# Kernel tuning notes

Hardware: AMD Instinct MI355X
Metric: run time of the kernel (lower is better)

The kernel has to match this reference:

```python
import jax, jax.numpy as jnp
import numpy as np

B, D, H, FPL, L, LOG2_T = 65536, 768, 512, 4, 16, 19
T = 2 ** LOG2_T
BASE_RES, FINEST_RES = 16, 512
PRIMES = jnp.array([1, 2654435761, 805459861], dtype=jnp.uint32)


def setup_inputs() -> dict:
    key = jax.random.key(0)
    ks = jax.random.split(key, 8)
    t = jax.random.uniform(ks[0], (B,), dtype=jnp.float32)
    x = jax.random.normal(ks[1], (B, D), dtype=jnp.float32)
    cond = jax.random.uniform(ks[2], (B, 2), dtype=jnp.float32)
    # one embedding table per level, Instant-NGP init U(-1e-4, 1e-4)
    tables = jax.random.uniform(ks[3], (L, T, FPL), dtype=jnp.float32,
                                minval=-1e-4, maxval=1e-4)
    in_dim = D + L * FPL  # 832

    def lin(k, fan_in, fan_out):
        return jax.random.normal(k, (fan_in, fan_out), dtype=jnp.float32) / np.sqrt(fan_in).astype(np.float32)

    W0, b0 = lin(ks[4], in_dim, H), jnp.zeros((H,), jnp.float32)
    W1, b1 = lin(ks[5], H, H), jnp.zeros((H,), jnp.float32)
    W2, b2 = lin(ks[6], H, H), jnp.zeros((H,), jnp.float32)
    W3, b3 = lin(ks[7], H, D), jnp.zeros((D,), jnp.float32)
    return dict(t=t, x=x, cond=cond, tables=tables,
                W0=W0, b0=b0, W1=W1, b1=b1, W2=W2, b2=b2, W3=W3, b3=b3)


def hash_encode(coords, tables):
    """coords: [B,3] in [0,1]; tables: [L,T,F] -> [B, L*F]."""
    Ln, Tn, Fn = tables.shape
    growth = np.exp((np.log(FINEST_RES) - np.log(BASE_RES)) / (Ln - 1))
    scales = jnp.asarray(np.floor(BASE_RES * growth ** np.arange(Ln)),
                         dtype=coords.dtype)                      # [L]
    xf = coords[:, None, :] * scales[None, :, None]               # [B,L,3]
    xl = jnp.floor(xf)
    w = xf - xl                                                   # [B,L,3] trilinear frac
    xi = xl.astype(jnp.uint32)
    # 8 cube-corner offsets
    offs = jnp.asarray(np.stack(np.meshgrid([0, 1], [0, 1], [0, 1],
                                            indexing='ij'), -1).reshape(8, 3),
                       dtype=jnp.uint32)                          # [8,3]
    corners = xi[:, :, None, :] + offs[None, None]                # [B,L,8,3]
    h = corners * PRIMES                                          # uint32 wraparound hash
    idx = (h[..., 0] ^ h[..., 1] ^ h[..., 2]) & jnp.uint32(Tn - 1)  # [B,L,8]
    feats = tables[jnp.arange(Ln)[None, :, None], idx]            # [B,L,8,F] gather
    offs_f = offs.astype(coords.dtype)
    wc = jnp.prod(jnp.where(offs_f[None, None] == 1,
                            w[:, :, None, :], 1 - w[:, :, None, :]), axis=-1)  # [B,L,8]
    out = jnp.einsum('blc,blcf->blf', wc, feats)                  # [B,L,F]
    return out.reshape(out.shape[0], Ln * Fn)


def reference(t, x, cond, tables, W0, b0, W1, b1, W2, b2, W3, b3):
    tcol = t[:, None] if t.ndim == 1 else t
    params3 = jnp.concatenate([cond, tcol], axis=-1)   # [B,3]
    enc = hash_encode(params3, tables)                  # [B,64]
    h = jnp.concatenate([x, enc], axis=-1)              # [B,832]
    h = jax.nn.silu(h @ W0 + b0)
    h = jax.nn.silu(h @ W1 + b1)
    h = jax.nn.silu(h @ W2 + b2)
    return h @ W3 + b3                                  # [B,768]
```

## Files before the change

kernel.cpp:

```cpp
#include <hip/hip_runtime.h>
#include <hip/hip_bf16.h>
#include <math.h>


#define T_SIZE 524288
#define T_MASK (T_SIZE - 1)

typedef _Float16 f16;
typedef _Float16 f16x8 __attribute__((ext_vector_type(8)));
typedef _Float16 f16x4 __attribute__((ext_vector_type(4)));
typedef float f32x4 __attribute__((ext_vector_type(4)));

struct Scales { float s[16]; };

__global__ void wfrag(const float* __restrict__ W, f16* __restrict__ Wf, int K, int N) {
  int tid = blockIdx.x * 256 + threadIdx.x;
  int lane = tid & 63, frag = tid >> 6;
  int KS = K >> 5;
  int nblk = frag / KS, ks = frag - nblk * KS;
  if (nblk * 16 >= N) return;
  int n = nblk * 16 + (lane & 15);
  int kb = ks * 32 + (lane >> 4) * 8;
  f16x8 v;
#pragma unroll
  for (int j = 0; j < 8; ++j) v[j] = (f16)W[(size_t)(kb + j) * N + n];
  *(f16x8*)(Wf + (size_t)frag * 512 + lane * 8) = v;
}

__device__ __forceinline__ float silu_f(float v) {
  return v * __builtin_amdgcn_rcpf(1.f + __expf(-v));
}

__global__ __launch_bounds__(512, 2) void fused_mlp(
    const float* __restrict__ x, const float* __restrict__ t,
    const float* __restrict__ cond, const float* __restrict__ tables,
    const f16* __restrict__ Wf0, const f16* __restrict__ Wf1,
    const f16* __restrict__ Wf2, const f16* __restrict__ Wf3,
    const float* __restrict__ b0, const float* __restrict__ b1,
    const float* __restrict__ b2, const float* __restrict__ b3,
    float* __restrict__ out, Scales scl) {
  __shared__ f16 act[128 * 512];
  __shared__ f16 stg[2 * 128 * 32];

  const int tid = threadIdx.x;
  const int wave = tid >> 6, lane = tid & 63;
  const int l16 = lane & 15, lhi = lane >> 4;
  const int rowBase = blockIdx.x * 128;
  const int sr = tid >> 2, sc = tid & 3;
  const int woff = sr * 32 + 8 * (sc ^ ((sr >> 1) & 3));

  f16x8 er24, er25;
  {
    int row = rowBase + sr;
    float c0 = cond[2 * row], c1 = cond[2 * row + 1], c2 = t[row];
#pragma unroll
    for (int h = 0; h < 2; ++h) {
      f16x8 er;
#pragma unroll
      for (int d = 0; d < 2; ++d) {
        int l = h * 8 + sc * 2 + d;
        float s = scl.s[l];
        float xf0 = c0 * s, xf1 = c1 * s, xf2 = c2 * s;
        float xl0 = floorf(xf0), xl1 = floorf(xf1), xl2 = floorf(xf2);
        float w0 = xf0 - xl0, w1 = xf1 - xl1, w2 = xf2 - xl2;
        unsigned xi0 = (unsigned)xl0, xi1 = (unsigned)xl1, xi2 = (unsigned)xl2;
        const float4* tl = (const float4*)tables + (size_t)l * T_SIZE;
        float a0 = 0.f, a1 = 0.f, a2 = 0.f, a3 = 0.f;
#pragma unroll
        for (int c = 0; c < 8; ++c) {
          unsigned ax = (c >> 2) & 1u, ay = (c >> 1) & 1u, az = c & 1u;
          unsigned hh = (xi0 + ax) ^ ((xi1 + ay) * 2654435761u) ^ ((xi2 + az) * 805459861u);
          float4 f = tl[hh & T_MASK];
          float wcw = (ax ? w0 : 1.f - w0) * (ay ? w1 : 1.f - w1) * (az ? w2 : 1.f - w2);
          a0 += wcw * f.x; a1 += wcw * f.y; a2 += wcw * f.z; a3 += wcw * f.w;
        }
        er[d * 4 + 0] = (f16)a0; er[d * 4 + 1] = (f16)a1;
        er[d * 4 + 2] = (f16)a2; er[d * 4 + 3] = (f16)a3;
      }
      if (h == 0) er24 = er; else er25 = er;
    }
  }

  f32x4 acc[8][4];
  f16x8 bfA[4], bfB[4], af[8];

#pragma unroll
  for (int mi = 0; mi < 8; ++mi)
#pragma unroll
    for (int ni = 0; ni < 4; ++ni) acc[mi][ni] = (f32x4){0.f, 0.f, 0.f, 0.f};

  {
    const float* xp = x + (size_t)(rowBase + sr) * 768 + sc * 8;
    float4 a = *(const float4*)xp, b = *(const float4*)(xp + 4);
    f16x8 v = { (f16)a.x, (f16)a.y, (f16)a.z, (f16)a.w,
                (f16)b.x, (f16)b.y, (f16)b.z, (f16)b.w };
    *(f16x8*)(stg + woff) = v;
  }
#pragma unroll
  for (int ni = 0; ni < 4; ++ni)
    bfA[ni] = *(const f16x8*)(Wf0 + ((size_t)(wave * 4 + ni) * 26) * 512 + lane * 8);
  __syncthreads();

#pragma unroll 1
  for (int ks = 0; ks < 26; ++ks) {
    const int nxt = ks + 1;
    f16x8 nv;
    if (nxt < 24) {
      const float* xp = x + (size_t)(rowBase + sr) * 768 + nxt * 32 + sc * 8;
      float4 a = *(const float4*)xp, b = *(const float4*)(xp + 4);
      nv = (f16x8){ (f16)a.x, (f16)a.y, (f16)a.z, (f16)a.w,
                    (f16)b.x, (f16)b.y, (f16)b.z, (f16)b.w };
    } else {
      nv = (nxt == 24) ? er24 : er25;
    }
    if (nxt < 26) {
#pragma unroll
      for (int ni = 0; ni < 4; ++ni)
        bfB[ni] = *(const f16x8*)(Wf0 + ((size_t)(wave * 4 + ni) * 26 + nxt) * 512 + lane * 8);
    }
    const int rb = (ks & 1) * 4096;
#pragma unroll
    for (int mi = 0; mi < 8; ++mi) {
      int r = mi * 16 + l16;
      af[mi] = *(const f16x8*)(stg + rb + r * 32 + 8 * (lhi ^ ((r >> 1) & 3)));
    }
    __builtin_amdgcn_s_setprio(1);
#pragma unroll
    for (int mi = 0; mi < 8; ++mi)
#pragma unroll
      for (int ni = 0; ni < 4; ++ni)
        acc[mi][ni] = __builtin_amdgcn_mfma_f32_16x16x32_f16(bfA[ni], af[mi], acc[mi][ni], 0, 0, 0);
    __builtin_amdgcn_s_setprio(0);
    if (nxt < 26) {
      *(f16x8*)(stg + (nxt & 1) * 4096 + woff) = nv;
#pragma unroll
      for (int ni = 0; ni < 4; ++ni) bfA[ni] = bfB[ni];
    }
    __syncthreads();
  }

  auto epi_act = [&](const float* __restrict__ bias) {
    __syncthreads();
#pragma unroll
    for (int mi = 0; mi < 8; ++mi) {
      const int row = mi * 16 + l16;
#pragma unroll
      for (int ni = 0; ni < 4; ++ni) {
        const int col = wave * 64 + ni * 16 + lhi * 4;
        float4 bv = *(const float4*)(bias + col);
        f16x4 o;
        o[0] = (f16)silu_f(acc[mi][ni][0] + bv.x);
        o[1] = (f16)silu_f(acc[mi][ni][1] + bv.y);
        o[2] = (f16)silu_f(acc[mi][ni][2] + bv.z);
        o[3] = (f16)silu_f(acc[mi][ni][3] + bv.w);
        *(f16x4*)(act + row * 512 + (col ^ ((row & 7) << 3))) = o;
      }
    }
    __syncthreads();
  };
  epi_act(b0);

  auto kloop4 = [&](const f16* __restrict__ Wf) {
#pragma unroll
    for (int mi = 0; mi < 8; ++mi)
#pragma unroll
      for (int ni = 0; ni < 4; ++ni) acc[mi][ni] = (f32x4){0.f, 0.f, 0.f, 0.f};
#pragma unroll
    for (int ni = 0; ni < 4; ++ni)
      bfA[ni] = *(const f16x8*)(Wf + ((size_t)(wave * 4 + ni) * 16) * 512 + lane * 8);
#pragma unroll 1
    for (int ks = 0; ks < 16; ++ks) {
      if (ks < 15) {
#pragma unroll
        for (int ni = 0; ni < 4; ++ni)
          bfB[ni] = *(const f16x8*)(Wf + ((size_t)(wave * 4 + ni) * 16 + ks + 1) * 512 + lane * 8);
      }
#pragma unroll
      for (int mi = 0; mi < 8; ++mi) {
        int r = mi * 16 + l16;
        af[mi] = *(const f16x8*)(act + r * 512 + ((ks * 32 + lhi * 8) ^ ((r & 7) << 3)));
      }
      __builtin_amdgcn_s_setprio(1);
#pragma unroll
      for (int mi = 0; mi < 8; ++mi)
#pragma unroll
        for (int ni = 0; ni < 4; ++ni)
          acc[mi][ni] = __builtin_amdgcn_mfma_f32_16x16x32_f16(bfA[ni], af[mi], acc[mi][ni], 0, 0, 0);
      __builtin_amdgcn_s_setprio(0);
      if (ks < 15) {
#pragma unroll
        for (int ni = 0; ni < 4; ++ni) bfA[ni] = bfB[ni];
      }
    }
  };

  kloop4(Wf1); epi_act(b1);
  kloop4(Wf2); epi_act(b2);

  kloop4(Wf3);
#pragma unroll
  for (int mi = 0; mi < 8; ++mi) {
    const size_t row = (size_t)(rowBase + mi * 16 + l16);
#pragma unroll
    for (int ni = 0; ni < 4; ++ni) {
      const int col = wave * 64 + ni * 16 + lhi * 4;
      float4 bv = *(const float4*)(b3 + col);
      float4 o = { acc[mi][ni][0] + bv.x, acc[mi][ni][1] + bv.y,
                   acc[mi][ni][2] + bv.z, acc[mi][ni][3] + bv.w };
      *(float4*)(out + row * 768 + col) = o;
    }
  }

#pragma unroll
  for (int mi = 0; mi < 8; ++mi)
#pragma unroll
    for (int ni = 0; ni < 2; ++ni) acc[mi][ni] = (f32x4){0.f, 0.f, 0.f, 0.f};
#pragma unroll
  for (int ni = 0; ni < 2; ++ni)
    bfA[ni] = *(const f16x8*)(Wf3 + ((size_t)(32 + wave * 2 + ni) * 16) * 512 + lane * 8);
#pragma unroll 1
  for (int ks = 0; ks < 16; ++ks) {
    if (ks < 15) {
#pragma unroll
      for (int ni = 0; ni < 2; ++ni)
        bfB[ni] = *(const f16x8*)(Wf3 + ((size_t)(32 + wave * 2 + ni) * 16 + ks + 1) * 512 + lane * 8);
    }
#pragma unroll
    for (int mi = 0; mi < 8; ++mi) {
      int r = mi * 16 + l16;
      af[mi] = *(const f16x8*)(act + r * 512 + ((ks * 32 + lhi * 8) ^ ((r & 7) << 3)));
    }
    __builtin_amdgcn_s_setprio(1);
#pragma unroll
    for (int mi = 0; mi < 8; ++mi)
#pragma unroll
      for (int ni = 0; ni < 2; ++ni)
        acc[mi][ni] = __builtin_amdgcn_mfma_f32_16x16x32_f16(bfA[ni], af[mi], acc[mi][ni], 0, 0, 0);
    __builtin_amdgcn_s_setprio(0);
    if (ks < 15) {
#pragma unroll
      for (int ni = 0; ni < 2; ++ni) bfA[ni] = bfB[ni];
    }
  }
#pragma unroll
  for (int mi = 0; mi < 8; ++mi) {
    const size_t row = (size_t)(rowBase + mi * 16 + l16);
#pragma unroll
    for (int ni = 0; ni < 2; ++ni) {
      const int col = 512 + wave * 32 + ni * 16 + lhi * 4;
      float4 bv = *(const float4*)(b3 + col);
      float4 o = { acc[mi][ni][0] + bv.x, acc[mi][ni][1] + bv.y,
                   acc[mi][ni][2] + bv.z, acc[mi][ni][3] + bv.w };
      *(float4*)(out + row * 768 + col) = o;
    }
  }
}

extern "C" void kernel_launch(void* const* d_in, const int* in_sizes, int n_in,
                              void* d_out, int out_size, void* d_ws, size_t ws_size,
                              hipStream_t stream) {
  const float* t    = (const float*)d_in[0];
  const float* x    = (const float*)d_in[1];
  const float* cond = (const float*)d_in[2];
  const float* tab  = (const float*)d_in[3];
  const float* W0   = (const float*)d_in[4];
  const float* b0   = (const float*)d_in[5];
  const float* W1   = (const float*)d_in[6];
  const float* b1   = (const float*)d_in[7];
  const float* W2   = (const float*)d_in[8];
  const float* b2   = (const float*)d_in[9];
  const float* W3   = (const float*)d_in[10];
  const float* b3   = (const float*)d_in[11];
  float* out = (float*)d_out;
  (void)in_sizes; (void)n_in; (void)out_size; (void)ws_size;

  char* ws = (char*)d_ws;
  f16* Wf0 = (f16*)(ws + 0);
  f16* Wf1 = (f16*)(ws + 851968);
  f16* Wf2 = (f16*)(ws + 1376256);
  f16* Wf3 = (f16*)(ws + 1900544);

  wfrag<<<dim3(208), 256, 0, stream>>>(W0, Wf0, 832, 512);
  wfrag<<<dim3(128), 256, 0, stream>>>(W1, Wf1, 512, 512);
  wfrag<<<dim3(128), 256, 0, stream>>>(W2, Wf2, 512, 512);
  wfrag<<<dim3(192), 256, 0, stream>>>(W3, Wf3, 512, 768);

  Scales sc;
  {
    double growth = exp((log(512.0) - log(16.0)) / 15.0);
    for (int l = 0; l < 16; ++l) sc.s[l] = (float)floor(16.0 * pow(growth, (double)l));
  }

  fused_mlp<<<dim3(512), 512, 0, stream>>>(x, t, cond, tab, Wf0, Wf1, Wf2, Wf3,
                                           b0, b1, b2, b3, out, sc);
}
```

Measured before the change: 305.2 us.

## Halve row tile to 64 per block to double grid and occupancy

```diff
diff --git a/kernel.cpp b/kernel.cpp
--- a/kernel.cpp
+++ b/kernel.cpp
@@ -31,7 +31,7 @@
   return v * __builtin_amdgcn_rcpf(1.f + __expf(-v));
 }
 
-__global__ __launch_bounds__(512, 2) void fused_mlp(
+__global__ __launch_bounds__(512, 4) void fused_mlp(
     const float* __restrict__ x, const float* __restrict__ t,
     const float* __restrict__ cond, const float* __restrict__ tables,
     const f16* __restrict__ Wf0, const f16* __restrict__ Wf1,
@@ -39,62 +39,54 @@
     const float* __restrict__ b0, const float* __restrict__ b1,
     const float* __restrict__ b2, const float* __restrict__ b3,
     float* __restrict__ out, Scales scl) {
-  __shared__ f16 act[128 * 512];
-  __shared__ f16 stg[2 * 128 * 32];
+  __shared__ f16 act[64 * 512];
+  __shared__ f16 stg[2 * 64 * 40];
 
   const int tid = threadIdx.x;
   const int wave = tid >> 6, lane = tid & 63;
   const int l16 = lane & 15, lhi = lane >> 4;
-  const int rowBase = blockIdx.x * 128;
-  const int sr = tid >> 2, sc = tid & 3;
-  const int woff = sr * 32 + 8 * (sc ^ ((sr >> 1) & 3));
-
-  f16x8 er24, er25;
+  const int rowBase = blockIdx.x * 64;
+  const int sr = tid >> 3, sc = tid & 7;
+
+  f16x4 er_a, er_b;
   {
     int row = rowBase + sr;
     float c0 = cond[2 * row], c1 = cond[2 * row + 1], c2 = t[row];
 #pragma unroll
     for (int h = 0; h < 2; ++h) {
-      f16x8 er;
-#pragma unroll
-      for (int d = 0; d < 2; ++d) {
-        int l = h * 8 + sc * 2 + d;
-        float s = scl.s[l];
-        float xf0 = c0 * s, xf1 = c1 * s, xf2 = c2 * s;
-        float xl0 = floorf(xf0), xl1 = floorf(xf1), xl2 = floorf(xf2);
-        float w0 = xf0 - xl0, w1 = xf1 - xl1, w2 = xf2 - xl2;
-        unsigned xi0 = (unsigned)xl0, xi1 = (unsigned)xl1, xi2 = (unsigned)xl2;
-        const float4* tl = (const float4*)tables + (size_t)l * T_SIZE;
-        float a0 = 0.f, a1 = 0.f, a2 = 0.f, a3 = 0.f;
-#pragma unroll
-        for (int c = 0; c < 8; ++c) {
-          unsigned ax = (c >> 2) & 1u, ay = (c >> 1) & 1u, az = c & 1u;
-          unsigned hh = (xi0 + ax) ^ ((xi1 + ay) * 2654435761u) ^ ((xi2 + az) * 805459861u);
-          float4 f = tl[hh & T_MASK];
-          float wcw = (ax ? w0 : 1.f - w0) * (ay ? w1 : 1.f - w1) * (az ? w2 : 1.f - w2);
-          a0 += wcw * f.x; a1 += wcw * f.y; a2 += wcw * f.z; a3 += wcw * f.w;
-        }
-        er[d * 4 + 0] = (f16)a0; er[d * 4 + 1] = (f16)a1;
-        er[d * 4 + 2] = (f16)a2; er[d * 4 + 3] = (f16)a3;
-      }
-      if (h == 0) er24 = er; else er25 = er;
-    }
-  }
-
-  f32x4 acc[8][4];
-  f16x8 bfA[4], bfB[4], af[8];
-
-#pragma unroll
-  for (int mi = 0; mi < 8; ++mi)
+      int l = sc + h * 8;
+      float s = scl.s[l];
+      float xf0 = c0 * s, xf1 = c1 * s, xf2 = c2 * s;
+      float xl0 = floorf(xf0), xl1 = floorf(xf1), xl2 = floorf(xf2);
+      float w0 = xf0 - xl0, w1 = xf1 - xl1, w2 = xf2 - xl2;
+      unsigned xi0 = (unsigned)xl0, xi1 = (unsigned)xl1, xi2 = (unsigned)xl2;
+      const float4* tl = (const float4*)tables + (size_t)l * T_SIZE;
+      float a0 = 0.f, a1 = 0.f, a2 = 0.f, a3 = 0.f;
+#pragma unroll
+      for (int c = 0; c < 8; ++c) {
+        unsigned ax = (c >> 2) & 1u, ay = (c >> 1) & 1u, az = c & 1u;
+        unsigned hh = (xi0 + ax) ^ ((xi1 + ay) * 2654435761u) ^ ((xi2 + az) * 805459861u);
+        float4 f = tl[hh & T_MASK];
+        float wcw = (ax ? w0 : 1.f - w0) * (ay ? w1 : 1.f - w1) * (az ? w2 : 1.f - w2);
+        a0 += wcw * f.x; a1 += wcw * f.y; a2 += wcw * f.z; a3 += wcw * f.w;
+      }
+      f16x4 er = { (f16)a0, (f16)a1, (f16)a2, (f16)a3 };
+      if (h == 0) er_a = er; else er_b = er;
+    }
+  }
+
+  f32x4 acc[4][4];
+  f16x8 bfA[4], bfB[4];
+
+#pragma unroll
+  for (int mi = 0; mi < 4; ++mi)
 #pragma unroll
     for (int ni = 0; ni < 4; ++ni) acc[mi][ni] = (f32x4){0.f, 0.f, 0.f, 0.f};
 
   {
-    const float* xp = x + (size_t)(rowBase + sr) * 768 + sc * 8;
-    float4 a = *(const float4*)xp, b = *(const float4*)(xp + 4);
-    f16x8 v = { (f16)a.x, (f16)a.y, (f16)a.z, (f16)a.w,
-                (f16)b.x, (f16)b.y, (f16)b.z, (f16)b.w };
-    *(f16x8*)(stg + woff) = v;
+    float4 a = *(const float4*)(x + (size_t)(rowBase + sr) * 768 + sc * 4);
+    f16x4 v = { (f16)a.x, (f16)a.y, (f16)a.z, (f16)a.w };
+    *(f16x4*)(stg + sr * 40 + sc * 4) = v;
   }
 #pragma unroll
   for (int ni = 0; ni < 4; ++ni)
@@ -104,35 +96,30 @@
 #pragma unroll 1
   for (int ks = 0; ks < 26; ++ks) {
     const int nxt = ks + 1;
-    f16x8 nv;
+    f16x4 nv;
     if (nxt < 24) {
-      const float* xp = x + (size_t)(rowBase + sr) * 768 + nxt * 32 + sc * 8;
-      float4 a = *(const float4*)xp, b = *(const float4*)(xp + 4);
-      nv = (f16x8){ (f16)a.x, (f16)a.y, (f16)a.z, (f16)a.w,
-                    (f16)b.x, (f16)b.y, (f16)b.z, (f16)b.w };
+      float4 a = *(const float4*)(x + (size_t)(rowBase + sr) * 768 + nxt * 32 + sc * 4);
+      nv = (f16x4){ (f16)a.x, (f16)a.y, (f16)a.z, (f16)a.w };
     } else {
-      nv = (nxt == 24) ? er24 : er25;
+      nv = (nxt == 24) ? er_a : er_b;
     }
     if (nxt < 26) {
 #pragma unroll
       for (int ni = 0; ni < 4; ++ni)
         bfB[ni] = *(const f16x8*)(Wf0 + ((size_t)(wave * 4 + ni) * 26 + nxt) * 512 + lane * 8);
     }
-    const int rb = (ks & 1) * 4096;
-#pragma unroll
-    for (int mi = 0; mi < 8; ++mi) {
-      int r = mi * 16 + l16;
-      af[mi] = *(const f16x8*)(stg + rb + r * 32 + 8 * (lhi ^ ((r >> 1) & 3)));
-    }
+    const f16* rb = stg + (ks & 1) * 2560;
     __builtin_amdgcn_s_setprio(1);
 #pragma unroll
-    for (int mi = 0; mi < 8; ++mi)
+    for (int mi = 0; mi < 4; ++mi) {
+      f16x8 af = *(const f16x8*)(rb + (mi * 16 + l16) * 40 + lhi * 8);
 #pragma unroll
       for (int ni = 0; ni < 4; ++ni)
-        acc[mi][ni] = __builtin_amdgcn_mfma_f32_16x16x32_f16(bfA[ni], af[mi], acc[mi][ni], 0, 0, 0);
+        acc[mi][ni] = __builtin_amdgcn_mfma_f32_16x16x32_f16(bfA[ni], af, acc[mi][ni], 0, 0, 0);
+    }
     __builtin_amdgcn_s_setprio(0);
     if (nxt < 26) {
-      *(f16x8*)(stg + (nxt & 1) * 4096 + woff) = nv;
+      *(f16x4*)(stg + (nxt & 1) * 2560 + sr * 40 + sc * 4) = nv;
 #pragma unroll
       for (int ni = 0; ni < 4; ++ni) bfA[ni] = bfB[ni];
     }
@@ -142,7 +129,7 @@
   auto epi_act = [&](const float* __restrict__ bias) {
     __syncthreads();
 #pragma unroll
-    for (int mi = 0; mi < 8; ++mi) {
+    for (int mi = 0; mi < 4; ++mi) {
       const int row = mi * 16 + l16;
 #pragma unroll
       for (int ni = 0; ni < 4; ++ni) {
@@ -162,7 +149,7 @@
 
   auto kloop4 = [&](const f16* __restrict__ Wf) {
 #pragma unroll
-    for (int mi = 0; mi < 8; ++mi)
+    for (int mi = 0; mi < 4; ++mi)
 #pragma unroll
       for (int ni = 0; ni < 4; ++ni) acc[mi][ni] = (f32x4){0.f, 0.f, 0.f, 0.f};
 #pragma unroll
@@ -175,17 +162,15 @@
         for (int ni = 0; ni < 4; ++ni)
           bfB[ni] = *(const f16x8*)(Wf + ((size_t)(wave * 4 + ni) * 16 + ks + 1) * 512 + lane * 8);
       }
-#pragma unroll
-      for (int mi = 0; mi < 8; ++mi) {
+      __builtin_amdgcn_s_setprio(1);
+#pragma unroll
+      for (int mi = 0; mi < 4; ++mi) {
         int r = mi * 16 + l16;
-        af[mi] = *(const f16x8*)(act + r * 512 + ((ks * 32 + lhi * 8) ^ ((r & 7) << 3)));
-      }
-      __builtin_amdgcn_s_setprio(1);
-#pragma unroll
-      for (int mi = 0; mi < 8; ++mi)
+        f16x8 af = *(const f16x8*)(act + r * 512 + ((ks * 32 + lhi * 8) ^ ((r & 7) << 3)));
 #pragma unroll
         for (int ni = 0; ni < 4; ++ni)
-          acc[mi][ni] = __builtin_amdgcn_mfma_f32_16x16x32_f16(bfA[ni], af[mi], acc[mi][ni], 0, 0, 0);
+          acc[mi][ni] = __builtin_amdgcn_mfma_f32_16x16x32_f16(bfA[ni], af, acc[mi][ni], 0, 0, 0);
+      }
       __builtin_amdgcn_s_setprio(0);
       if (ks < 15) {
 #pragma unroll
@@ -199,7 +184,7 @@
 
   kloop4(Wf3);
 #pragma unroll
-  for (int mi = 0; mi < 8; ++mi) {
+  for (int mi = 0; mi < 4; ++mi) {
     const size_t row = (size_t)(rowBase + mi * 16 + l16);
 #pragma unroll
     for (int ni = 0; ni < 4; ++ni) {
@@ -212,7 +197,7 @@
   }
 
 #pragma unroll
-  for (int mi = 0; mi < 8; ++mi)
+  for (int mi = 0; mi < 4; ++mi)
 #pragma unroll
     for (int ni = 0; ni < 2; ++ni) acc[mi][ni] = (f32x4){0.f, 0.f, 0.f, 0.f};
 #pragma unroll
@@ -225,17 +210,15 @@
       for (int ni = 0; ni < 2; ++ni)
         bfB[ni] = *(const f16x8*)(Wf3 + ((size_t)(32 + wave * 2 + ni) * 16 + ks + 1) * 512 + lane * 8);
     }
-#pragma unroll
-    for (int mi = 0; mi < 8; ++mi) {
+    __builtin_amdgcn_s_setprio(1);
+#pragma unroll
+    for (int mi = 0; mi < 4; ++mi) {
       int r = mi * 16 + l16;
-      af[mi] = *(const f16x8*)(act + r * 512 + ((ks * 32 + lhi * 8) ^ ((r & 7) << 3)));
-    }
-    __builtin_amdgcn_s_setprio(1);
-#pragma unroll
-    for (int mi = 0; mi < 8; ++mi)
+      f16x8 af = *(const f16x8*)(act + r * 512 + ((ks * 32 + lhi * 8) ^ ((r & 7) << 3)));
 #pragma unroll
       for (int ni = 0; ni < 2; ++ni)
-        acc[mi][ni] = __builtin_amdgcn_mfma_f32_16x16x32_f16(bfA[ni], af[mi], acc[mi][ni], 0, 0, 0);
+        acc[mi][ni] = __builtin_amdgcn_mfma_f32_16x16x32_f16(bfA[ni], af, acc[mi][ni], 0, 0, 0);
+    }
     __builtin_amdgcn_s_setprio(0);
     if (ks < 15) {
 #pragma unroll
@@ -243,7 +226,7 @@
     }
   }
 #pragma unroll
-  for (int mi = 0; mi < 8; ++mi) {
+  for (int mi = 0; mi < 4; ++mi) {
     const size_t row = (size_t)(rowBase + mi * 16 + l16);
 #pragma unroll
     for (int ni = 0; ni < 2; ++ni) {
@@ -291,6 +274,6 @@
     for (int l = 0; l < 16; ++l) sc.s[l] = (float)floor(16.0 * pow(growth, (double)l));
   }
 
-  fused_mlp<<<dim3(512), 512, 0, stream>>>(x, t, cond, tab, Wf0, Wf1, Wf2, Wf3,
-                                           b0, b1, b2, b3, out, sc);
-}
+  fused_mlp<<<dim3(1024), 512, 0, stream>>>(x, t, cond, tab, Wf0, Wf1, Wf2, Wf3,
+                                            b0, b1, b2, b3, out, sc);
+}
```

After: 309.3 us. No clear change (+1.3%).
